# Optimization experiments

Measured on AMD Instinct MI355X. Metric: run time of the kernel, lower is better.

Reference implementation:

```python
import jax, jax.numpy as jnp
import numpy as np

T, B, I, H = 2048, 64, 256, 256

def setup_inputs() -> dict:
    key = jax.random.key(0)
    k_x, k_wih, k_whh = jax.random.split(key, 3)
    x = jax.random.normal(k_x, (T, B, I), dtype=jnp.float32)
    h0 = jnp.zeros((1, B, H), dtype=jnp.float32)
    # nn.RNN weight_ih_l0 init: U(-1/sqrt(H), 1/sqrt(H)); shape [H, I]
    bound = 1.0 / np.sqrt(H)
    W_ih = jax.random.uniform(k_wih, (H, I), minval=-bound, maxval=bound, dtype=jnp.float32)
    # IndRNN recurrent weight: diagonal vector, U(-1, 1); biases are zeroed.
    w_hh = jax.random.uniform(k_whh, (H,), minval=-1.0, maxval=1.0, dtype=jnp.float32)
    return {"x": x, "h0": h0, "W_ih": W_ih, "w_hh": w_hh}

def reference(x, h0, W_ih, w_hh):
    # Precompute the input projection for all timesteps (the only GEMM):
    # [T, B, H] = x @ W_ih^T  (biases are zero)
    xW = jnp.einsum('tbi,hi->tbh', x, W_ih)

    def step(h, xw_t):
        # IndRNN: diagonal recurrence -> elementwise multiply instead of matmul
        h_new = jax.nn.relu(xw_t + h * w_hh)
        return h_new, h_new

    h_last, outputs = jax.lax.scan(step, h0[0], xW)
    return outputs, h_last[None]  # ([T,B,H], [1,B,H]) matching nn.RNN
```

## Files before the change

### kernel.cpp

```cpp
#include <hip/hip_runtime.h>

typedef short v8s __attribute__((ext_vector_type(8)));
typedef float v4f __attribute__((ext_vector_type(4)));

#define BATCH 16
#define NBATCH 128
#define BH 16384
#define TBH 33554432

__device__ __forceinline__ ushort f2bf(float f) {
  uint u = __float_as_uint(f);
  u += 0x7FFF + ((u >> 16) & 1);
  return (ushort)(u >> 16);
}

__global__ __launch_bounds__(512) void indrnn_gemm(
    const float* __restrict__ A,
    const float* __restrict__ W,
    ushort* __restrict__ C)
{
  __shared__ ushort As[128 * 72];
  __shared__ ushort Bs[256 * 72];

  const int tid  = threadIdx.x;
  const int lane = tid & 63;
  const int wid  = tid >> 6;
  const int wm   = wid >> 2;
  const int wn   = wid & 3;
  const int m0   = blockIdx.x * 128;

  const int l15 = lane & 15;
  const int lhi = lane >> 4;

  v4f acc[4][4] = {};

  for (int kc = 0; kc < 4; ++kc) {
    #pragma unroll
    for (int j = 0; j < 4; ++j) {
      int f    = j * 512 + tid;
      int row  = f >> 4;
      int colf = f & 15;
      const float4 a4 = *(const float4*)(A + ((size_t)(m0 + row) << 8) + kc * 64 + colf * 4);
      ushort4 b4 = make_ushort4(f2bf(a4.x), f2bf(a4.y), f2bf(a4.z), f2bf(a4.w));
      *(ushort4*)(As + row * 72 + colf * 4) = b4;
    }
    #pragma unroll
    for (int j = 0; j < 8; ++j) {
      int f    = j * 512 + tid;
      int row  = f >> 4;
      int colf = f & 15;
      const float4 a4 = *(const float4*)(W + ((size_t)row << 8) + kc * 64 + colf * 4);
      ushort4 b4 = make_ushort4(f2bf(a4.x), f2bf(a4.y), f2bf(a4.z), f2bf(a4.w));
      *(ushort4*)(Bs + row * 72 + colf * 4) = b4;
    }
    __syncthreads();

    #pragma unroll
    for (int kk = 0; kk < 2; ++kk) {
      const int koff = kk * 32 + lhi * 8;
      v8s af[4], bf[4];
      #pragma unroll
      for (int mt = 0; mt < 4; ++mt)
        af[mt] = *(const v8s*)(As + (wm * 64 + mt * 16 + l15) * 72 + koff);
      #pragma unroll
      for (int nt = 0; nt < 4; ++nt)
        bf[nt] = *(const v8s*)(Bs + (wn * 64 + nt * 16 + l15) * 72 + koff);
      #pragma unroll
      for (int mt = 0; mt < 4; ++mt)
        #pragma unroll
        for (int nt = 0; nt < 4; ++nt)
          acc[mt][nt] = __builtin_amdgcn_mfma_f32_16x16x32_bf16(af[mt], bf[nt], acc[mt][nt], 0, 0, 0);
    }
    __syncthreads();
  }

  #pragma unroll
  for (int mt = 0; mt < 4; ++mt) {
    #pragma unroll
    for (int nt = 0; nt < 4; ++nt) {
      #pragma unroll
      for (int r = 0; r < 4; ++r) {
        int row = m0 + wm * 64 + mt * 16 + lhi * 4 + r;
        int col = wn * 64 + nt * 16 + l15;
        C[((size_t)row << 8) + col] = f2bf(acc[mt][nt][r]);
      }
    }
  }
}

__global__ __launch_bounds__(64) void indrnn_scan(
    const ushort* __restrict__ xw,
    const float* __restrict__ h0,
    const float* __restrict__ w_hh,
    float* __restrict__ out)
{
  const int ch = blockIdx.x * 64 + threadIdx.x;
  const float w = w_hh[ch & 255];
  float h = h0[ch];
  const ushort* px = xw + ch;
  float* po = out + ch;

  uint b0[BATCH], b1[BATCH], b2[BATCH], b3[BATCH];

  auto ld = [&](uint (&buf)[BATCH], int kb) {
    const ushort* p = px + (size_t)kb * BATCH * BH;
    #pragma unroll
    for (int j = 0; j < BATCH; ++j) buf[j] = p[(size_t)j * BH];
  };
  auto cp = [&](uint (&buf)[BATCH], int kb) {
    float* o = po + (size_t)kb * BATCH * BH;
    #pragma unroll
    for (int j = 0; j < BATCH; ++j) {
      float xv = __uint_as_float(buf[j] << 16);
      h = fmaxf(fmaf(h, w, xv), 0.0f);
      o[(size_t)j * BH] = h;
    }
  };

  ld(b0, 0); ld(b1, 1); ld(b2, 2); ld(b3, 3);
  for (int kb = 0; kb < NBATCH; kb += 4) {
    cp(b0, kb);     if (kb + 4 < NBATCH) ld(b0, kb + 4);
    cp(b1, kb + 1); if (kb + 5 < NBATCH) ld(b1, kb + 5);
    cp(b2, kb + 2); if (kb + 6 < NBATCH) ld(b2, kb + 6);
    cp(b3, kb + 3); if (kb + 7 < NBATCH) ld(b3, kb + 7);
  }
  out[(size_t)TBH + ch] = h;
}

extern "C" void kernel_launch(void* const* d_in, const int* in_sizes, int n_in,
                              void* d_out, int out_size, void* d_ws, size_t ws_size,
                              hipStream_t stream) {
  const float* x    = (const float*)d_in[0];
  const float* h0   = (const float*)d_in[1];
  const float* W_ih = (const float*)d_in[2];
  const float* w_hh = (const float*)d_in[3];
  float* out = (float*)d_out;
  ushort* xw = (ushort*)d_ws;

  indrnn_gemm<<<dim3(1024), dim3(512), 0, stream>>>(x, W_ih, xw);
  indrnn_scan<<<dim3(256), dim3(64), 0, stream>>>(xw, h0, w_hh, out);
}
```

Before: 297.5 us.

## Keep W_ih fragments in registers and stream A directly without LDS

The GEMM kernel is restructured so each wave keeps its 64-column slice of W_ih converted to bf16 in registers for the whole block. A rows are loaded straight from global memory into MFMA fragment layout, with the next 16-row chunk prefetched while the current one computes. This removes the shared-memory staging, the per-chunk reloading and reconverting of W, and the __syncthreads barriers. Packed bf16 conversion via v_cvt_pk_bf16_f32 replaces scalar rounding. The cost is heavy register pressure (128 VGPRs of weights plus prefetch buffers) and uncoalesced per-lane global loads of A.

```diff
diff --git a/kernel.cpp b/kernel.cpp
--- a/kernel.cpp
+++ b/kernel.cpp
@@ -14,76 +14,102 @@
   return (ushort)(u >> 16);
 }
 
-__global__ __launch_bounds__(512) void indrnn_gemm(
+__device__ __forceinline__ uint pkbf2(float a, float b) {
+  uint r;
+  asm("v_cvt_pk_bf16_f32 %0, %1, %2" : "=v"(r) : "v"(a), "v"(b));
+  return r;
+}
+
+union frag_u { uint u[4]; v8s s; };
+
+__global__ __launch_bounds__(256, 2) void indrnn_gemm(
     const float* __restrict__ A,
     const float* __restrict__ W,
     ushort* __restrict__ C)
 {
-  __shared__ ushort As[128 * 72];
-  __shared__ ushort Bs[256 * 72];
-
   const int tid  = threadIdx.x;
   const int lane = tid & 63;
-  const int wid  = tid >> 6;
-  const int wm   = wid >> 2;
-  const int wn   = wid & 3;
-  const int m0   = blockIdx.x * 128;
+  const int wv   = tid >> 6;
+  const int l15  = lane & 15;
+  const int lhi  = lane >> 4;
+  const int c0   = wv * 64;
+  const int rowblk = blockIdx.x * 256;
 
-  const int l15 = lane & 15;
-  const int lhi = lane >> 4;
+  frag_u wfr[4][8];
+  #pragma unroll
+  for (int nt = 0; nt < 4; ++nt) {
+    const float* pw = W + (((size_t)(c0 + nt * 16 + l15)) << 8) + (lhi << 3);
+    #pragma unroll
+    for (int kk = 0; kk < 8; ++kk) {
+      const float4 w0 = *(const float4*)(pw + kk * 32);
+      const float4 w1 = *(const float4*)(pw + kk * 32 + 4);
+      wfr[nt][kk].u[0] = pkbf2(w0.x, w0.y);
+      wfr[nt][kk].u[1] = pkbf2(w0.z, w0.w);
+      wfr[nt][kk].u[2] = pkbf2(w1.x, w1.y);
+      wfr[nt][kk].u[3] = pkbf2(w1.z, w1.w);
+    }
+  }
 
-  v4f acc[4][4] = {};
+  const float* pA = A + (((size_t)(rowblk + l15)) << 8) + (lhi << 3);
 
-  for (int kc = 0; kc < 4; ++kc) {
-    #pragma unroll
-    for (int j = 0; j < 4; ++j) {
-      int f    = j * 512 + tid;
-      int row  = f >> 4;
-      int colf = f & 15;
-      const float4 a4 = *(const float4*)(A + ((size_t)(m0 + row) << 8) + kc * 64 + colf * 4);
-      ushort4 b4 = make_ushort4(f2bf(a4.x), f2bf(a4.y), f2bf(a4.z), f2bf(a4.w));
-      *(ushort4*)(As + row * 72 + colf * 4) = b4;
-    }
-    #pragma unroll
-    for (int j = 0; j < 8; ++j) {
-      int f    = j * 512 + tid;
-      int row  = f >> 4;
-      int colf = f & 15;
-      const float4 a4 = *(const float4*)(W + ((size_t)row << 8) + kc * 64 + colf * 4);
-      ushort4 b4 = make_ushort4(f2bf(a4.x), f2bf(a4.y), f2bf(a4.z), f2bf(a4.w));
-      *(ushort4*)(Bs + row * 72 + colf * 4) = b4;
-    }
-    __syncthreads();
+  float4 fa[8], fb[8];
+  #pragma unroll
+  for (int kk = 0; kk < 4; ++kk) {
+    fa[2*kk]   = *(const float4*)(pA + kk * 32);
+    fa[2*kk+1] = *(const float4*)(pA + kk * 32 + 4);
+    fb[2*kk]   = *(const float4*)(pA + 128 + kk * 32);
+    fb[2*kk+1] = *(const float4*)(pA + 128 + kk * 32 + 4);
+  }
+
+  for (int c = 0; c < 16; ++c) {
+    v4f acc[4] = {};
+    const float* pAn = pA + (size_t)(c + 1) * 4096;
 
     #pragma unroll
-    for (int kk = 0; kk < 2; ++kk) {
-      const int koff = kk * 32 + lhi * 8;
-      v8s af[4], bf[4];
-      #pragma unroll
-      for (int mt = 0; mt < 4; ++mt)
-        af[mt] = *(const v8s*)(As + (wm * 64 + mt * 16 + l15) * 72 + koff);
+    for (int kk = 0; kk < 4; ++kk) {
+      frag_u af;
+      af.u[0] = pkbf2(fa[2*kk].x,   fa[2*kk].y);
+      af.u[1] = pkbf2(fa[2*kk].z,   fa[2*kk].w);
+      af.u[2] = pkbf2(fa[2*kk+1].x, fa[2*kk+1].y);
+      af.u[3] = pkbf2(fa[2*kk+1].z, fa[2*kk+1].w);
       #pragma unroll
       for (int nt = 0; nt < 4; ++nt)
-        bf[nt] = *(const v8s*)(Bs + (wn * 64 + nt * 16 + l15) * 72 + koff);
+        acc[nt] = __builtin_amdgcn_mfma_f32_16x16x32_bf16(af.s, wfr[nt][kk].s, acc[nt], 0, 0, 0);
+    }
+    if (c + 1 < 16) {
       #pragma unroll
-      for (int mt = 0; mt < 4; ++mt)
-        #pragma unroll
-        for (int nt = 0; nt < 4; ++nt)
-          acc[mt][nt] = __builtin_amdgcn_mfma_f32_16x16x32_bf16(af[mt], bf[nt], acc[mt][nt], 0, 0, 0);
+      for (int kk = 0; kk < 4; ++kk) {
+        fa[2*kk]   = *(const float4*)(pAn + kk * 32);
+        fa[2*kk+1] = *(const float4*)(pAn + kk * 32 + 4);
+      }
     }
-    __syncthreads();
-  }
 
-  #pragma unroll
-  for (int mt = 0; mt < 4; ++mt) {
+    #pragma unroll
+    for (int kk = 0; kk < 4; ++kk) {
+      frag_u af;
+      af.u[0] = pkbf2(fb[2*kk].x,   fb[2*kk].y);
+      af.u[1] = pkbf2(fb[2*kk].z,   fb[2*kk].w);
+      af.u[2] = pkbf2(fb[2*kk+1].x, fb[2*kk+1].y);
+      af.u[3] = pkbf2(fb[2*kk+1].z, fb[2*kk+1].w);
+      #pragma unroll
+      for (int nt = 0; nt < 4; ++nt)
+        acc[nt] = __builtin_amdgcn_mfma_f32_16x16x32_bf16(af.s, wfr[nt][kk + 4].s, acc[nt], 0, 0, 0);
+    }
+    if (c + 1 < 16) {
+      #pragma unroll
+      for (int kk = 0; kk < 4; ++kk) {
+        fb[2*kk]   = *(const float4*)(pAn + 128 + kk * 32);
+        fb[2*kk+1] = *(const float4*)(pAn + 128 + kk * 32 + 4);
+      }
+    }
+
+    const int mrow = rowblk + c * 16 + lhi * 4;
     #pragma unroll
     for (int nt = 0; nt < 4; ++nt) {
+      const int col = c0 + nt * 16 + l15;
       #pragma unroll
-      for (int r = 0; r < 4; ++r) {
-        int row = m0 + wm * 64 + mt * 16 + lhi * 4 + r;
-        int col = wn * 64 + nt * 16 + l15;
-        C[((size_t)row << 8) + col] = f2bf(acc[mt][nt][r]);
-      }
+      for (int r = 0; r < 4; ++r)
+        C[(((size_t)(mrow + r)) << 8) + col] = f2bf(acc[nt][r]);
     }
   }
 }
@@ -137,6 +163,6 @@
   float* out = (float*)d_out;
   ushort* xw = (ushort*)d_ws;
 
-  indrnn_gemm<<<dim3(1024), dim3(512), 0, stream>>>(x, W_ih, xw);
+  indrnn_gemm<<<dim3(512), dim3(256), 0, stream>>>(x, W_ih, xw);
   indrnn_scan<<<dim3(256), dim3(64), 0, stream>>>(xw, h0, w_hh, out);
 }
```

Measured after the change: 321.1 us. 1.08x slower.

## Warp-specialize scan with producer wave staging xW tiles into LDS via async loads

Applied to the files above, without the earlier changes.

The scan kernel gains a second wavefront per block that acts as a producer. It prefetches 128-timestep tiles of the bf16 projection into a triple-buffered LDS ring using global_load_lds. The consumer wave reads from LDS and runs the serial recurrence, so global load latency should overlap with the dependent compute chain. This replaces the per-thread register prefetch of 64 strided loads. It adds a block barrier per tile and relies on hand-written vmcnt waits being correct.

```diff
diff --git a/kernel.cpp b/kernel.cpp
--- a/kernel.cpp
+++ b/kernel.cpp
@@ -3,10 +3,10 @@
 typedef short v8s __attribute__((ext_vector_type(8)));
 typedef float v4f __attribute__((ext_vector_type(4)));
 
-#define BATCH 16
-#define NBATCH 128
 #define BH 16384
 #define TBH 33554432
+#define SCAN_TILE 128
+#define NTILE 16
 
 __device__ __forceinline__ ushort f2bf(float f) {
   uint u = __float_as_uint(f);
@@ -88,43 +88,75 @@
   }
 }
 
-__global__ __launch_bounds__(64) void indrnn_scan(
+__global__ __launch_bounds__(128) void indrnn_scan(
     const ushort* __restrict__ xw,
     const float* __restrict__ h0,
     const float* __restrict__ w_hh,
     float* __restrict__ out)
 {
-  const int ch = blockIdx.x * 64 + threadIdx.x;
-  const float w = w_hh[ch & 255];
-  float h = h0[ch];
-  const ushort* px = xw + ch;
-  float* po = out + ch;
+  __shared__ __align__(16) ushort tile[3][SCAN_TILE * 64];
 
-  uint b0[BATCH], b1[BATCH], b2[BATCH], b3[BATCH];
+  const int lane = threadIdx.x & 63;
+  const int wv   = threadIdx.x >> 6;
+  const int ch0  = blockIdx.x * 64;
+  const int ch   = ch0 + lane;
 
-  auto ld = [&](uint (&buf)[BATCH], int kb) {
-    const ushort* p = px + (size_t)kb * BATCH * BH;
+  const size_t psrc0 = (size_t)(lane >> 3) * BH + (size_t)ch0 + ((lane & 7) << 3);
+
+  auto stage = [&](int ti) {
+    const ushort* src = xw + (size_t)ti * SCAN_TILE * BH + psrc0;
+    ushort* dst = &tile[ti % 3][0];
     #pragma unroll
-    for (int j = 0; j < BATCH; ++j) buf[j] = p[(size_t)j * BH];
-  };
-  auto cp = [&](uint (&buf)[BATCH], int kb) {
-    float* o = po + (size_t)kb * BATCH * BH;
-    #pragma unroll
-    for (int j = 0; j < BATCH; ++j) {
-      float xv = __uint_as_float(buf[j] << 16);
-      h = fmaxf(fmaf(h, w, xv), 0.0f);
-      o[(size_t)j * BH] = h;
+    for (int j = 0; j < 16; ++j) {
+      __builtin_amdgcn_global_load_lds(
+          (const float*)(src + (size_t)j * 8 * BH),
+          (float*)(dst + j * 512), 16, 0, 0);
     }
   };
 
-  ld(b0, 0); ld(b1, 1); ld(b2, 2); ld(b3, 3);
-  for (int kb = 0; kb < NBATCH; kb += 4) {
-    cp(b0, kb);     if (kb + 4 < NBATCH) ld(b0, kb + 4);
-    cp(b1, kb + 1); if (kb + 5 < NBATCH) ld(b1, kb + 5);
-    cp(b2, kb + 2); if (kb + 6 < NBATCH) ld(b2, kb + 6);
-    cp(b3, kb + 3); if (kb + 7 < NBATCH) ld(b3, kb + 7);
+  float h = 0.0f, w = 0.0f;
+  if (wv == 0) {
+    h = h0[ch];
+    w = w_hh[ch & 255];
+  } else {
+    stage(0);
+    stage(1);
+    asm volatile("s_waitcnt vmcnt(16)" ::: "memory");
   }
-  out[(size_t)TBH + ch] = h;
+  asm volatile("" ::: "memory");
+  __builtin_amdgcn_s_barrier();
+  __builtin_amdgcn_sched_barrier(0);
+
+  for (int i = 0; i < NTILE; ++i) {
+    if (wv == 0) {
+      const ushort* tp = &tile[i % 3][lane];
+      float* po = out + (size_t)i * SCAN_TILE * BH + ch;
+      #pragma unroll
+      for (int t = 0; t < SCAN_TILE; t += 16) {
+        ushort v[16];
+        #pragma unroll
+        for (int j = 0; j < 16; ++j) v[j] = tp[(t + j) * 64];
+        #pragma unroll
+        for (int j = 0; j < 16; ++j) {
+          float xv = __uint_as_float((uint)v[j] << 16);
+          h = fmaxf(fmaf(h, w, xv), 0.0f);
+          po[(size_t)(t + j) * BH] = h;
+        }
+      }
+    } else {
+      if (i + 2 < NTILE) {
+        stage(i + 2);
+        asm volatile("s_waitcnt vmcnt(16)" ::: "memory");
+      } else {
+        asm volatile("s_waitcnt vmcnt(0)" ::: "memory");
+      }
+    }
+    asm volatile("" ::: "memory");
+    __builtin_amdgcn_s_barrier();
+    __builtin_amdgcn_sched_barrier(0);
+  }
+
+  if (wv == 0) out[(size_t)TBH + ch] = h;
 }
 
 extern "C" void kernel_launch(void* const* d_in, const int* in_sizes, int n_in,
@@ -138,5 +170,5 @@
   ushort* xw = (ushort*)d_ws;
 
   indrnn_gemm<<<dim3(1024), dim3(512), 0, stream>>>(x, W_ih, xw);
-  indrnn_scan<<<dim3(256), dim3(64), 0, stream>>>(xw, h0, w_hh, out);
+  indrnn_scan<<<dim3(256), dim3(128), 0, stream>>>(xw, h0, w_hh, out);
 }
```

Result: no change. 298.6 us (+0.4%).
